# Optimization experiments

Measured on AMD Instinct MI355X. Metric: run time of the kernel, lower is better.

## Reference

```python
import jax, jax.numpy as jnp
import numpy as np

EPS = 1e-5
BLOCK = 16

def setup_inputs() -> dict:
    key = jax.random.key(0)
    ks = jax.random.split(key, 5)
    B, S, D = 8, 4096, 1024
    G = D // BLOCK            # 64 groups
    sq = int(np.sqrt(D))      # 32
    x = jax.random.normal(ks[0], (B, S, D), dtype=jnp.float32)
    gamma = jnp.ones((D,), jnp.float32)
    beta = jnp.zeros((D,), jnp.float32)
    block_weights = 0.5 * jax.random.normal(ks[1], (G, BLOCK, BLOCK), dtype=jnp.float32)
    W_row = 0.1 * jax.random.normal(ks[2], (sq, sq), dtype=jnp.float32)
    W_col = 0.1 * jax.random.normal(ks[3], (sq, sq), dtype=jnp.float32)
    alpha = jnp.float32(0.3)
    bias = jnp.zeros((D,), jnp.float32)
    return {"x": x, "gamma": gamma, "beta": beta, "block_weights": block_weights,
            "W_row": W_row, "W_col": W_col, "alpha": alpha, "bias": bias}

def reference(x, gamma, beta, block_weights, W_row, W_col, alpha, bias):
    D = x.shape[-1]
    G, Bk, _ = block_weights.shape      # 64, 16, 16 (D == G*Bk, no pad)
    sq = W_row.shape[0]                 # 32 (D == sq*sq, no pad)
    # LayerNorm (fp32)
    mu = jnp.mean(x, axis=-1, keepdims=True)
    var = jnp.mean(jnp.square(x - mu), axis=-1, keepdims=True)
    xn = (x - mu) * jax.lax.rsqrt(var + EPS) * gamma + beta
    x_flat = xn.reshape(-1, D)          # [N, D]
    # Block-diagonal mix: [N, G, Bk] x [G, Bk, Bk]
    xg = x_flat.reshape(-1, G, Bk)
    y = jnp.einsum('ngb,gbc->ngc', xg, block_weights).reshape(-1, D)
    block_out = jnp.flip(y, axis=-1)
    # Monarch path: [N, sq, sq] @ W_col @ W_row^T
    xgrid = x_flat.reshape(-1, sq, sq)
    z = jnp.einsum('nrc,ck,sk->nrs', xgrid, W_col, W_row).reshape(-1, D)
    out = block_out + alpha * z + bias
    return out.reshape(x.shape)
```

## Files before the change

### kernel.cpp

```cpp
#include <hip/hip_runtime.h>

typedef __bf16 bf16x8 __attribute__((ext_vector_type(8)));
typedef __bf16 bf16x4 __attribute__((ext_vector_type(4)));
typedef float f32x4 __attribute__((ext_vector_type(4)));

#define EPS 1e-5f

__global__ __launch_bounds__(256) void hbsl_precompute(
    const float* __restrict__ bw, const float* __restrict__ W_row,
    const float* __restrict__ W_col, const float* __restrict__ alpha_p,
    __bf16* __restrict__ mt, __bf16* __restrict__ bwt)
{
    const int t = threadIdx.x;
    if (blockIdx.x == 0) {
        const float alpha = alpha_p[0];
        #pragma unroll
        for (int k = 0; k < 4; ++k) {
            int flat = t + 256 * k;
            int s = flat >> 5, c = flat & 31;
            float acc = 0.f;
            #pragma unroll 8
            for (int kk = 0; kk < 32; ++kk)
                acc += W_col[c * 32 + kk] * W_row[s * 32 + kk];
            mt[s * 32 + c] = (__bf16)(alpha * acc);
        }
    } else {
        int g = blockIdx.x - 1;
        int c = t >> 4, b = t & 15;
        bwt[g * 256 + c * 16 + b] = (__bf16)bw[g * 256 + b * 16 + c];
    }
}

__global__ __launch_bounds__(256, 4) void hbsl_main(
    const float* __restrict__ x, const float* __restrict__ gamma,
    const float* __restrict__ beta, const float* __restrict__ bias,
    const __bf16* __restrict__ mt, const __bf16* __restrict__ bwt,
    float* __restrict__ out)
{
    __shared__ __bf16 xn[16 * 1032];
    __shared__ float bias_s[1024];
    const int t = threadIdx.x;
    const int lane = t & 63;
    const int wv = t >> 6;
    const int q = lane >> 4, n = lane & 15;
    const int row = t >> 4, li = t & 15;
    const int rbase = blockIdx.x * 16;

    bf16x8 mfrag0 = *(const bf16x8*)(mt + n * 32 + q * 8);
    bf16x8 mfrag1 = *(const bf16x8*)(mt + (16 + n) * 32 + q * 8);

    bf16x8 bwf[8];
    #pragma unroll
    for (int p = 0; p < 8; ++p) {
        const int o0 = wv * 16 + 2 * p;
        const int gp = 31 - (o0 >> 1);
        const int g = (q >= 2) ? (2 * gp + 1) : (2 * gp);
        const int e = (q >= 2) ? (q - 2) * 8 : q * 8;
        bwf[p] = *(const bf16x8*)(bwt + g * 256 + (15 - n) * 16 + e);
    }

    *(float4*)(&bias_s[t * 4]) = *(const float4*)(bias + t * 4);

    const float* xr = x + (size_t)(rbase + row) * 1024;
    float4 xv[16];
    float s = 0.f, ss = 0.f;
    #pragma unroll
    for (int i = 0; i < 16; ++i) {
        xv[i] = *(const float4*)(xr + li * 4 + i * 64);
        s += xv[i].x + xv[i].y + xv[i].z + xv[i].w;
        ss += xv[i].x * xv[i].x + xv[i].y * xv[i].y
            + xv[i].z * xv[i].z + xv[i].w * xv[i].w;
    }
    #pragma unroll
    for (int m = 1; m < 16; m <<= 1) {
        s  += __shfl_xor(s, m, 64);
        ss += __shfl_xor(ss, m, 64);
    }
    const float mu = s * (1.f / 1024.f);
    const float rstd = rsqrtf(ss * (1.f / 1024.f) - mu * mu + EPS);
    #pragma unroll
    for (int i = 0; i < 16; ++i) {
        const int col = li * 4 + i * 64;
        float4 g4 = *(const float4*)(gamma + col);
        float4 b4 = *(const float4*)(beta + col);
        bf16x4 v;
        v[0] = (__bf16)((xv[i].x - mu) * rstd * g4.x + b4.x);
        v[1] = (__bf16)((xv[i].y - mu) * rstd * g4.y + b4.y);
        v[2] = (__bf16)((xv[i].z - mu) * rstd * g4.z + b4.z);
        v[3] = (__bf16)((xv[i].w - mu) * rstd * g4.w + b4.w);
        *(bf16x4*)(&xn[row * 1032 + col]) = v;
    }
    __syncthreads();

    bf16x8 bz;
    #pragma unroll
    for (int i = 0; i < 8; ++i) bz[i] = (__bf16)0.f;
    const f32x4 zf = {0.f, 0.f, 0.f, 0.f};

    #pragma unroll
    for (int p = 0; p < 8; ++p) {
        const int o0 = wv * 16 + 2 * p;
        const int r  = o0 >> 1;
        const int gp = 31 - r;

        bf16x8 az = *(const bf16x8*)(&xn[n * 1032 + r  * 32 + q * 8]);
        bf16x8 ay = *(const bf16x8*)(&xn[n * 1032 + gp * 32 + q * 8]);

        bf16x8 a0 = (q >= 2) ? bwf[p] : bz;
        bf16x8 a1 = (q <  2) ? bwf[p] : bz;

        f32x4 z0 = __builtin_amdgcn_mfma_f32_16x16x32_bf16(mfrag0, az, zf, 0, 0, 0);
        f32x4 z1 = __builtin_amdgcn_mfma_f32_16x16x32_bf16(mfrag1, az, zf, 0, 0, 0);
        f32x4 y0 = __builtin_amdgcn_mfma_f32_16x16x32_bf16(a0, ay, zf, 0, 0, 0);
        f32x4 y1 = __builtin_amdgcn_mfma_f32_16x16x32_bf16(a1, ay, zf, 0, 0, 0);

        f32x4 b0 = *(const f32x4*)(&bias_s[o0 * 16 + q * 4]);
        f32x4 b1 = *(const f32x4*)(&bias_s[o0 * 16 + 16 + q * 4]);

        float* op = out + (size_t)(rbase + n) * 1024 + o0 * 16 + q * 4;
        *(f32x4*)op        = y0 + z0 + b0;
        *(f32x4*)(op + 16) = y1 + z1 + b1;
    }
}

extern "C" void kernel_launch(void* const* d_in, const int* in_sizes, int n_in,
                              void* d_out, int out_size, void* d_ws, size_t ws_size,
                              hipStream_t stream) {
    const float* x      = (const float*)d_in[0];
    const float* gamma  = (const float*)d_in[1];
    const float* beta   = (const float*)d_in[2];
    const float* bw     = (const float*)d_in[3];
    const float* W_row  = (const float*)d_in[4];
    const float* W_col  = (const float*)d_in[5];
    const float* alpha  = (const float*)d_in[6];
    const float* bias   = (const float*)d_in[7];
    float* o = (float*)d_out;

    __bf16* mt  = (__bf16*)d_ws;
    __bf16* bwt = (__bf16*)((char*)d_ws + 2048);

    const int N = in_sizes[0] / 1024;

    hipLaunchKernelGGL(hbsl_precompute, dim3(65), dim3(256), 0, stream,
                       bw, W_row, W_col, alpha, mt, bwt);
    hipLaunchKernelGGL(hbsl_main, dim3(N / 16), dim3(256), 0, stream,
                       x, gamma, beta, bias, mt, bwt, o);
}
```

Baseline: 258.2 us.

## Fold LayerNorm affine terms into precomputed linear-map constants, apply stats post-MFMA

Uses the linearity of the block-diagonal and Monarch maps to move the mean/rstd normalization after the MFMAs. Each row's x*gamma is written to LDS during the single stats pass, so the float4 x array no longer has to stay live in registers. The precompute kernel builds L(gamma) and L(beta)+bias constants, and the epilogue applies rstd*(y+z) - mu*rstd*L(gamma) + c2. This shortens the register-heavy prologue and removes the second x pass. In exchange, un-centered values are rounded to bf16 before the MFMAs, which risks precision loss (cancellation) when the mean is large.

```diff
diff --git a/kernel.cpp b/kernel.cpp
--- a/kernel.cpp
+++ b/kernel.cpp
@@ -3,17 +3,41 @@
 typedef __bf16 bf16x8 __attribute__((ext_vector_type(8)));
 typedef __bf16 bf16x4 __attribute__((ext_vector_type(4)));
 typedef float f32x4 __attribute__((ext_vector_type(4)));
+typedef float f32x2 __attribute__((ext_vector_type(2)));
 
 #define EPS 1e-5f
 
+
+__device__ float apply_L(const float* __restrict__ v, const float* __restrict__ bw,
+                         const float* __restrict__ W_row, const float* __restrict__ W_col,
+                         float alpha, int dp) {
+    const int f = 1023 - dp, g = f >> 4, c = f & 15;
+    float yb = 0.f;
+    #pragma unroll
+    for (int b = 0; b < 16; ++b) yb += v[g * 16 + b] * bw[g * 256 + b * 16 + c];
+    const int r = dp >> 5, s = dp & 31;
+    float zm = 0.f;
+    #pragma unroll 4
+    for (int k = 0; k < 32; ++k) {
+        float tmp = 0.f;
+        #pragma unroll 8
+        for (int cc = 0; cc < 32; ++cc) tmp += v[r * 32 + cc] * W_col[cc * 32 + k];
+        zm += tmp * W_row[s * 32 + k];
+    }
+    return yb + alpha * zm;
+}
+
 __global__ __launch_bounds__(256) void hbsl_precompute(
+    const float* __restrict__ gamma, const float* __restrict__ beta,
     const float* __restrict__ bw, const float* __restrict__ W_row,
     const float* __restrict__ W_col, const float* __restrict__ alpha_p,
-    __bf16* __restrict__ mt, __bf16* __restrict__ bwt)
+    const float* __restrict__ bias,
+    __bf16* __restrict__ mt, __bf16* __restrict__ bwt,
+    __bf16* __restrict__ lgc, __bf16* __restrict__ c2)
 {
     const int t = threadIdx.x;
+    const float alpha = alpha_p[0];
     if (blockIdx.x == 0) {
-        const float alpha = alpha_p[0];
         #pragma unroll
         for (int k = 0; k < 4; ++k) {
             int flat = t + 256 * k;
@@ -24,21 +48,35 @@
                 acc += W_col[c * 32 + kk] * W_row[s * 32 + kk];
             mt[s * 32 + c] = (__bf16)(alpha * acc);
         }
-    } else {
+    } else if (blockIdx.x <= 64) {
         int g = blockIdx.x - 1;
         int c = t >> 4, b = t & 15;
         bwt[g * 256 + c * 16 + b] = (__bf16)bw[g * 256 + b * 16 + c];
+    } else if (blockIdx.x == 65) {
+        #pragma unroll
+        for (int k = 0; k < 4; ++k) {
+            int dp = t + 256 * k;
+            lgc[dp] = (__bf16)apply_L(gamma, bw, W_row, W_col, alpha, dp);
+        }
+    } else {
+        #pragma unroll
+        for (int k = 0; k < 4; ++k) {
+            int dp = t + 256 * k;
+            c2[dp] = (__bf16)(apply_L(beta, bw, W_row, W_col, alpha, dp) + bias[dp]);
+        }
     }
 }
 
 __global__ __launch_bounds__(256, 4) void hbsl_main(
     const float* __restrict__ x, const float* __restrict__ gamma,
-    const float* __restrict__ beta, const float* __restrict__ bias,
     const __bf16* __restrict__ mt, const __bf16* __restrict__ bwt,
+    const __bf16* __restrict__ lgc, const __bf16* __restrict__ c2,
     float* __restrict__ out)
 {
     __shared__ __bf16 xn[16 * 1032];
-    __shared__ float bias_s[1024];
+    __shared__ __bf16 lgc_s[1024];
+    __shared__ __bf16 c2_s[1024];
+    __shared__ float stats_s[32];
     const int t = threadIdx.x;
     const int lane = t & 63;
     const int wv = t >> 6;
@@ -48,7 +86,6 @@
 
     bf16x8 mfrag0 = *(const bf16x8*)(mt + n * 32 + q * 8);
     bf16x8 mfrag1 = *(const bf16x8*)(mt + (16 + n) * 32 + q * 8);
-
     bf16x8 bwf[8];
     #pragma unroll
     for (int p = 0; p < 8; ++p) {
@@ -58,18 +95,24 @@
         const int e = (q >= 2) ? (q - 2) * 8 : q * 8;
         bwf[p] = *(const bf16x8*)(bwt + g * 256 + (15 - n) * 16 + e);
     }
-
-    *(float4*)(&bias_s[t * 4]) = *(const float4*)(bias + t * 4);
+    *(bf16x4*)(&lgc_s[t * 4]) = *(const bf16x4*)(lgc + t * 4);
+    *(bf16x4*)(&c2_s[t * 4])  = *(const bf16x4*)(c2 + t * 4);
 
     const float* xr = x + (size_t)(rbase + row) * 1024;
-    float4 xv[16];
     float s = 0.f, ss = 0.f;
     #pragma unroll
     for (int i = 0; i < 16; ++i) {
-        xv[i] = *(const float4*)(xr + li * 4 + i * 64);
-        s += xv[i].x + xv[i].y + xv[i].z + xv[i].w;
-        ss += xv[i].x * xv[i].x + xv[i].y * xv[i].y
-            + xv[i].z * xv[i].z + xv[i].w * xv[i].w;
+        const int col = li * 4 + i * 64;
+        float4 xv = *(const float4*)(xr + col);
+        float4 g4 = *(const float4*)(gamma + col);
+        s += xv.x + xv.y + xv.z + xv.w;
+        ss += xv.x * xv.x + xv.y * xv.y + xv.z * xv.z + xv.w * xv.w;
+        bf16x4 v;
+        v[0] = (__bf16)(xv.x * g4.x);
+        v[1] = (__bf16)(xv.y * g4.y);
+        v[2] = (__bf16)(xv.z * g4.z);
+        v[3] = (__bf16)(xv.w * g4.w);
+        *(bf16x4*)(&xn[row * 1032 + col]) = v;
     }
     #pragma unroll
     for (int m = 1; m < 16; m <<= 1) {
@@ -78,17 +121,9 @@
     }
     const float mu = s * (1.f / 1024.f);
     const float rstd = rsqrtf(ss * (1.f / 1024.f) - mu * mu + EPS);
-    #pragma unroll
-    for (int i = 0; i < 16; ++i) {
-        const int col = li * 4 + i * 64;
-        float4 g4 = *(const float4*)(gamma + col);
-        float4 b4 = *(const float4*)(beta + col);
-        bf16x4 v;
-        v[0] = (__bf16)((xv[i].x - mu) * rstd * g4.x + b4.x);
-        v[1] = (__bf16)((xv[i].y - mu) * rstd * g4.y + b4.y);
-        v[2] = (__bf16)((xv[i].z - mu) * rstd * g4.z + b4.z);
-        v[3] = (__bf16)((xv[i].w - mu) * rstd * g4.w + b4.w);
-        *(bf16x4*)(&xn[row * 1032 + col]) = v;
+    if (li == 0) {
+        stats_s[row * 2]     = rstd;
+        stats_s[row * 2 + 1] = -mu * rstd;
     }
     __syncthreads();
 
@@ -96,6 +131,8 @@
     #pragma unroll
     for (int i = 0; i < 8; ++i) bz[i] = (__bf16)0.f;
     const f32x4 zf = {0.f, 0.f, 0.f, 0.f};
+
+    const f32x2 st = *(const f32x2*)(&stats_s[n * 2]);
 
     #pragma unroll
     for (int p = 0; p < 8; ++p) {
@@ -114,12 +151,20 @@
         f32x4 y0 = __builtin_amdgcn_mfma_f32_16x16x32_bf16(a0, ay, zf, 0, 0, 0);
         f32x4 y1 = __builtin_amdgcn_mfma_f32_16x16x32_bf16(a1, ay, zf, 0, 0, 0);
 
-        f32x4 b0 = *(const f32x4*)(&bias_s[o0 * 16 + q * 4]);
-        f32x4 b1 = *(const f32x4*)(&bias_s[o0 * 16 + 16 + q * 4]);
+        bf16x4 lg0 = *(const bf16x4*)(&lgc_s[o0 * 16 + q * 4]);
+        bf16x4 lg1 = *(const bf16x4*)(&lgc_s[o0 * 16 + 16 + q * 4]);
+        bf16x4 cc0 = *(const bf16x4*)(&c2_s[o0 * 16 + q * 4]);
+        bf16x4 cc1 = *(const bf16x4*)(&c2_s[o0 * 16 + 16 + q * 4]);
 
+        f32x4 r0, r1;
+        #pragma unroll
+        for (int e = 0; e < 4; ++e) {
+            r0[e] = fmaf(y0[e] + z0[e], st[0], fmaf((float)lg0[e], st[1], (float)cc0[e]));
+            r1[e] = fmaf(y1[e] + z1[e], st[0], fmaf((float)lg1[e], st[1], (float)cc1[e]));
+        }
         float* op = out + (size_t)(rbase + n) * 1024 + o0 * 16 + q * 4;
-        *(f32x4*)op        = y0 + z0 + b0;
-        *(f32x4*)(op + 16) = y1 + z1 + b1;
+        *(f32x4*)op        = r0;
+        *(f32x4*)(op + 16) = r1;
     }
 }
 
@@ -138,11 +183,13 @@
 
     __bf16* mt  = (__bf16*)d_ws;
     __bf16* bwt = (__bf16*)((char*)d_ws + 2048);
+    __bf16* lgc = (__bf16*)((char*)d_ws + 34816);
+    __bf16* c2  = (__bf16*)((char*)d_ws + 36864);
 
     const int N = in_sizes[0] / 1024;
 
-    hipLaunchKernelGGL(hbsl_precompute, dim3(65), dim3(256), 0, stream,
-                       bw, W_row, W_col, alpha, mt, bwt);
+    hipLaunchKernelGGL(hbsl_precompute, dim3(67), dim3(256), 0, stream,
+                       gamma, beta, bw, W_row, W_col, alpha, bias, mt, bwt, lgc, c2);
     hipLaunchKernelGGL(hbsl_main, dim3(N / 16), dim3(256), 0, stream,
-                       x, gamma, beta, bias, mt, bwt, o);
+                       x, gamma, mt, bwt, lgc, c2, o);
 }
```

Result: slower. 309.5 us (+19.9%).
